# Optimization experiments

Measured on AMD Instinct MI355X. Metric: run time of the kernel, lower is better.

## Reference

```python
import jax, jax.numpy as jnp
import numpy as np

B, S, D_IN, H, G, HD = 1, 2048, 2048, 32, 8, 128
GS = H // G  # group_size = 4
D_OUT = H * HD  # 4096
EPS = 1e-6


def _rmsnorm(x, scale):
    # qwen3-compatible: compute in fp32 over last dim
    xf = x.astype(jnp.float32)
    var = jnp.mean(xf * xf, axis=-1, keepdims=True)
    return (xf * jax.lax.rsqrt(var + EPS) * scale).astype(x.dtype)


def _apply_rope(x, cos, sin):
    # x: [b, h, s, d]; cos/sin: [s, d]
    d2 = x.shape[-1] // 2
    x1, x2 = x[..., :d2], x[..., d2:]
    rotated = jnp.concatenate([-x2, x1], axis=-1)
    return (x * cos[None, None] + rotated * sin[None, None]).astype(x.dtype)


def setup_inputs() -> dict:
    key = jax.random.key(0)
    ks = jax.random.split(key, 8)
    x = jax.random.normal(ks[0], (B, S, D_IN), jnp.float32)
    mask = jnp.triu(jnp.ones((S, S), bool), k=1)  # causal: True = masked
    # RoPE tables [S, HD]
    inv_freq = 1.0 / (10000.0 ** (jnp.arange(0, HD, 2, dtype=jnp.float32) / HD))
    ang = jnp.arange(S, dtype=jnp.float32)[:, None] * inv_freq[None, :]
    ang = jnp.concatenate([ang, ang], axis=-1)
    cos, sin = jnp.cos(ang), jnp.sin(ang)
    std = 0.02
    Wq = jax.random.normal(ks[1], (D_IN, D_OUT), jnp.float32) * std
    Wk = jax.random.normal(ks[2], (D_IN, G * HD), jnp.float32) * std
    Wv = jax.random.normal(ks[3], (D_IN, G * HD), jnp.float32) * std
    Wo = jax.random.normal(ks[4], (D_OUT, D_IN), jnp.float32) * std
    q_scale = jnp.ones((HD,), jnp.float32)
    k_scale = jnp.ones((HD,), jnp.float32)
    return {"x": x, "mask": mask, "cos": cos, "sin": sin,
            "Wq": Wq, "Wk": Wk, "Wv": Wv, "Wo": Wo,
            "q_scale": q_scale, "k_scale": k_scale}


def reference(x, mask, cos, sin, Wq, Wk, Wv, Wo, q_scale, k_scale):
    b, s, _ = x.shape
    q = (x @ Wq).reshape(b, s, H, HD).transpose(0, 2, 1, 3)   # [b,H,s,hd]
    k = (x @ Wk).reshape(b, s, G, HD).transpose(0, 2, 1, 3)   # [b,G,s,hd]
    v = (x @ Wv).reshape(b, s, G, HD).transpose(0, 2, 1, 3)   # [b,G,s,hd]
    q = _rmsnorm(q, q_scale)
    k = _rmsnorm(k, k_scale)
    q = _apply_rope(q, cos[:s], sin[:s])
    k = _apply_rope(k, cos[:s], sin[:s])
    next_k, next_v = k, v  # cache (num_kv_groups heads)
    # GQA via broadcasting instead of repeat_interleave (same math)
    qg = q.reshape(b, G, GS, s, HD)
    scores = jnp.einsum('bgrsd,bgtd->bgrst', qg, k)           # [b,G,gs,s,s]
    scores = jnp.where(mask[None, None, None], -jnp.inf, scores)
    attn = jax.nn.softmax(scores / np.sqrt(HD).astype(np.float32), axis=-1)
    ctx = jnp.einsum('bgrst,bgtd->bgrsd', attn, v)            # [b,G,gs,s,hd]
    ctx = ctx.reshape(b, H, s, HD).transpose(0, 2, 1, 3).reshape(b, s, D_OUT)
    out = ctx @ Wo
    return out, next_k, next_v
```

## Files before the change

kernel.cpp:

```cpp
#include <hip/hip_runtime.h>

typedef unsigned short ushort_t;
typedef short short8 __attribute__((ext_vector_type(8)));
typedef float floatx4 __attribute__((ext_vector_type(4)));

#define S_LEN 2048
#define DIN   2048
#define NH    32
#define NG    8
#define HDIM  128
#define DOUT  4096
#define DKV   1024
#define QLD   6144

__device__ __forceinline__ float b2f(ushort_t u) {
  union { float f; unsigned u; } t; t.u = ((unsigned)u) << 16; return t.f;
}
__device__ __forceinline__ ushort_t f2b(float f) {
  union { float f; unsigned u; } t; t.f = f;
  unsigned v = t.u;
  v += 0x7FFFu + ((v >> 16) & 1u);
  return (ushort_t)(v >> 16);
}

__device__ __forceinline__ void glds16(const ushort_t* g, ushort_t* l) {
  __builtin_amdgcn_global_load_lds((const __attribute__((address_space(1))) void*)g,
                                   (__attribute__((address_space(3))) void*)l, 16, 0, 0);
}

__global__ __launch_bounds__(256) void tcastW(const float* __restrict__ Wq,
                                              const float* __restrict__ Wk,
                                              const float* __restrict__ Wv,
                                              ushort_t* __restrict__ Wt) {
  __shared__ float t[32][33];
  const int x = blockIdx.x;
  const float* W; int N, sx, drow;
  if (x < 128)      { W = Wq; N = DOUT; sx = x * 32;         drow = x * 32; }
  else if (x < 160) { W = Wk; N = DKV;  sx = (x - 128) * 32; drow = 4096 + (x - 128) * 32; }
  else              { W = Wv; N = DKV;  sx = (x - 160) * 32; drow = 5120 + (x - 160) * 32; }
  const int by = blockIdx.y * 32;
  const int tx = threadIdx.x & 31;
  const int ty = threadIdx.x >> 5;
#pragma unroll
  for (int i = 0; i < 32; i += 8)
    t[ty + i][tx] = W[(size_t)(by + ty + i) * N + sx + tx];
  __syncthreads();
#pragma unroll
  for (int i = 0; i < 32; i += 8)
    Wt[(size_t)(drow + ty + i) * DIN + by + tx] = f2b(t[tx][ty + i]);
}

__global__ __launch_bounds__(256) void tcast(const float* __restrict__ W,
                                             ushort_t* __restrict__ Wt,
                                             int N, int ldt) {
  __shared__ float t[32][33];
  const int bx = blockIdx.x * 32;
  const int by = blockIdx.y * 32;
  const int tx = threadIdx.x & 31;
  const int ty = threadIdx.x >> 5;
#pragma unroll
  for (int i = 0; i < 32; i += 8)
    t[ty + i][tx] = W[(size_t)(by + ty + i) * N + bx + tx];
  __syncthreads();
#pragma unroll
  for (int i = 0; i < 32; i += 8)
    Wt[(size_t)(bx + ty + i) * ldt + by + tx] = f2b(t[tx][ty + i]);
}

__global__ __launch_bounds__(256) void castx(const float* __restrict__ x,
                                             ushort_t* __restrict__ xb) {
  const size_t i = ((size_t)blockIdx.x * 256 + threadIdx.x) * 4;
  float4 v = *(const float4*)&x[i];
  union { int2 p; ushort_t s[4]; } w;
  w.s[0] = f2b(v.x); w.s[1] = f2b(v.y); w.s[2] = f2b(v.z); w.s[3] = f2b(v.w);
  *(int2*)&xb[i] = w.p;
}

template <int CF32, int BM>
__global__ __launch_bounds__(256) void gemm_glds(const ushort_t* __restrict__ A, int lda,
                                                 const ushort_t* __restrict__ Bt, int ldb,
                                                 void* __restrict__ Cp, int ldc, int K) {
  constexpr int MI = BM / 32;
  __shared__ __align__(16) ushort_t As[3][BM * 32];
  __shared__ __align__(16) ushort_t Bs[3][4096];
  const int tid  = threadIdx.x;
  const int m0   = blockIdx.y * BM;
  const int n0   = blockIdx.x * 128;
  const int wave = tid >> 6, lane = tid & 63;
  const int lrow = lane & 15, quad = lane >> 4;
  const int wm = (wave >> 1) * (BM / 2), wn = (wave & 1) * 64;

  floatx4 acc[MI][4];
#pragma unroll
  for (int mi = 0; mi < MI; mi++)
#pragma unroll
    for (int ni = 0; ni < 4; ni++)
#pragma unroll
      for (int j = 0; j < 4; j++) acc[mi][ni][j] = 0.0f;

  const int sc = ((tid & 3) ^ ((tid >> 3) & 3)) * 8;
  const ushort_t* ag0 = A + (size_t)(m0 + (tid >> 2)) * lda + sc;
  const ushort_t* ag1 = ag0 + (size_t)64 * lda;
  const ushort_t* bg0 = Bt + (size_t)(n0 + (tid >> 2)) * ldb + sc;
  const ushort_t* bg1 = bg0 + (size_t)64 * ldb;
  const int so = wave * 512;

  auto stage = [&](int k0, ushort_t* aB, ushort_t* bB) {
    glds16(ag0 + k0, aB + so);
    if constexpr (BM == 128) glds16(ag1 + k0, aB + 2048 + so);
    glds16(bg0 + k0, bB + so);
    glds16(bg1 + k0, bB + 2048 + so);
  };

  const int rq = (quad ^ ((lrow >> 1) & 3)) * 8;

  stage(0,  As[0], Bs[0]);
  stage(32, As[1], Bs[1]);
  stage(64, As[2], Bs[2]);

  ushort_t *a_cur = As[0], *a_n1 = As[1], *a_n2 = As[2];
  ushort_t *b_cur = Bs[0], *b_n1 = Bs[1], *b_n2 = Bs[2];

  const int NT = K >> 5;
  for (int t = 0; t < NT; t++) {
    if (t + 2 < NT) {
      if constexpr (BM == 128) asm volatile("s_waitcnt vmcnt(8)" ::: "memory");
      else                     asm volatile("s_waitcnt vmcnt(6)" ::: "memory");
    } else if (t + 1 < NT) {
      if constexpr (BM == 128) asm volatile("s_waitcnt vmcnt(4)" ::: "memory");
      else                     asm volatile("s_waitcnt vmcnt(3)" ::: "memory");
    } else {
      asm volatile("s_waitcnt vmcnt(0)" ::: "memory");
    }
    __builtin_amdgcn_s_barrier();

    short8 af[MI], bfr[4];
#pragma unroll
    for (int mi = 0; mi < MI; mi++)
      af[mi] = *(const short8*)&a_cur[(wm + mi * 16 + lrow) * 32 + rq];
#pragma unroll
    for (int ni = 0; ni < 4; ni++)
      bfr[ni] = *(const short8*)&b_cur[(wn + ni * 16 + lrow) * 32 + rq];
    asm volatile("s_waitcnt lgkmcnt(0)" ::: "memory");
    __builtin_amdgcn_s_barrier();

    if (t + 3 < NT) stage((t + 3) << 5, a_cur, b_cur);

    __builtin_amdgcn_s_setprio(1);
#pragma unroll
    for (int mi = 0; mi < MI; mi++)
#pragma unroll
      for (int ni = 0; ni < 4; ni++)
        acc[mi][ni] = __builtin_amdgcn_mfma_f32_16x16x32_bf16(af[mi], bfr[ni], acc[mi][ni], 0, 0, 0);
    __builtin_amdgcn_s_setprio(0);

    ushort_t* ta = a_cur; a_cur = a_n1; a_n1 = a_n2; a_n2 = ta;
    ushort_t* tb = b_cur; b_cur = b_n1; b_n1 = b_n2; b_n2 = tb;
  }
  asm volatile("s_waitcnt vmcnt(0)" ::: "memory");

#pragma unroll
  for (int mi = 0; mi < MI; mi++)
#pragma unroll
    for (int ni = 0; ni < 4; ni++)
#pragma unroll
      for (int i = 0; i < 4; i++) {
        const int row = m0 + wm + mi * 16 + quad * 4 + i;
        const int col = n0 + wn + ni * 16 + lrow;
        if (CF32) ((float*)Cp)[(size_t)row * ldc + col] = acc[mi][ni][i];
        else      ((ushort_t*)Cp)[(size_t)row * ldc + col] = f2b(acc[mi][ni][i]);
      }
}

__global__ __launch_bounds__(256, 2) void gemm_o(const ushort_t* __restrict__ A, int lda,
                                                 const ushort_t* __restrict__ Bt, int ldb,
                                                 float* __restrict__ C, int ldc, int K) {
  __shared__ __align__(16) ushort_t As[3][64 * 64];
  __shared__ __align__(16) ushort_t Bs[3][128 * 64];
  const int tid  = threadIdx.x;
  const int m0   = blockIdx.y * 64;
  const int n0   = blockIdx.x * 128;
  const int wave = tid >> 6, lane = tid & 63;
  const int lrow = lane & 15, quad = lane >> 4;
  const int wm = (wave >> 1) * 32, wn = (wave & 1) * 64;

  floatx4 acc[2][4];
#pragma unroll
  for (int mi = 0; mi < 2; mi++)
#pragma unroll
    for (int ni = 0; ni < 4; ni++)
#pragma unroll
      for (int j = 0; j < 4; j++) acc[mi][ni][j] = 0.0f;

  const int sc = ((lane & 7) ^ ((lane >> 3) & 7)) * 8;
  const ushort_t* ag = A  + (size_t)(m0 + wave * 8 + (lane >> 3)) * lda + sc;
  const ushort_t* bg = Bt + (size_t)(n0 + wave * 8 + (lane >> 3)) * ldb + sc;

  auto stage = [&](int k0, ushort_t* aB, ushort_t* bB) {
    glds16(ag + k0,                    aB + wave * 512);
    glds16(ag + (size_t)32 * lda + k0, aB + 2048 + wave * 512);
    glds16(bg + k0,                    bB + wave * 512);
    glds16(bg + (size_t)32 * ldb + k0, bB + 2048 + wave * 512);
    glds16(bg + (size_t)64 * ldb + k0, bB + 4096 + wave * 512);
    glds16(bg + (size_t)96 * ldb + k0, bB + 6144 + wave * 512);
  };

  const int rq0 = ((quad)     ^ (lrow & 7)) * 8;
  const int rq1 = ((4 + quad) ^ (lrow & 7)) * 8;

  stage(0,   As[0], Bs[0]);
  stage(64,  As[1], Bs[1]);
  stage(128, As[2], Bs[2]);

  ushort_t *a_cur = As[0], *a_n1 = As[1], *a_n2 = As[2];
  ushort_t *b_cur = Bs[0], *b_n1 = Bs[1], *b_n2 = Bs[2];

  const int NT = K >> 6;
  for (int t = 0; t < NT; t++) {
    if (t + 2 < NT)      asm volatile("s_waitcnt vmcnt(12)" ::: "memory");
    else if (t + 1 < NT) asm volatile("s_waitcnt vmcnt(6)" ::: "memory");
    else                 asm volatile("s_waitcnt vmcnt(0)" ::: "memory");
    __builtin_amdgcn_s_barrier();

    short8 af[2][2], bfr[2][4];
#pragma unroll
    for (int mi = 0; mi < 2; mi++) {
      af[0][mi] = *(const short8*)&a_cur[(wm + mi * 16 + lrow) * 64 + rq0];
      af[1][mi] = *(const short8*)&a_cur[(wm + mi * 16 + lrow) * 64 + rq1];
    }
#pragma unroll
    for (int ni = 0; ni < 4; ni++) {
      bfr[0][ni] = *(const short8*)&b_cur[(wn + ni * 16 + lrow) * 64 + rq0];
      bfr[1][ni] = *(const short8*)&b_cur[(wn + ni * 16 + lrow) * 64 + rq1];
    }
    asm volatile("s_waitcnt lgkmcnt(0)" ::: "memory");
    __builtin_amdgcn_s_barrier();

    if (t + 3 < NT) stage((t + 3) << 6, a_cur, b_cur);

    __builtin_amdgcn_s_setprio(1);
#pragma unroll
    for (int kd = 0; kd < 2; kd++)
#pragma unroll
      for (int mi = 0; mi < 2; mi++)
#pragma unroll
        for (int ni = 0; ni < 4; ni++)
          acc[mi][ni] = __builtin_amdgcn_mfma_f32_16x16x32_bf16(af[kd][mi], bfr[kd][ni], acc[mi][ni], 0, 0, 0);
    __builtin_amdgcn_s_setprio(0);

    ushort_t* ta = a_cur; a_cur = a_n1; a_n1 = a_n2; a_n2 = ta;
    ushort_t* tb = b_cur; b_cur = b_n1; b_n1 = b_n2; b_n2 = tb;
  }
  asm volatile("s_waitcnt vmcnt(0)" ::: "memory");

#pragma unroll
  for (int mi = 0; mi < 2; mi++)
#pragma unroll
    for (int ni = 0; ni < 4; ni++)
#pragma unroll
      for (int i = 0; i < 4; i++) {
        const int row = m0 + wm + mi * 16 + quad * 4 + i;
        const int col = n0 + wn + ni * 16 + lrow;
        C[(size_t)row * ldc + col] = acc[mi][ni][i];
      }
}

__global__ __launch_bounds__(256) void norm_qk(ushort_t* __restrict__ qkv,
                                               const float* __restrict__ cosb,
                                               const float* __restrict__ sinb,
                                               const float* __restrict__ qs,
                                               const float* __restrict__ ks,
                                               ushort_t* __restrict__ kb) {
  const int idx  = blockIdx.x * 4 + (threadIdx.x >> 6);
  const int lane = threadIdx.x & 63;
  const int SH = S_LEN * NH;
  const float QSC = 0.08838834764831845f * 1.4426950408889634f;

  if (idx < SH) {
    const int s = idx >> 5, h = idx & 31;
    ushort_t* row = qkv + (size_t)s * QLD + h * HDIM;
    float x1 = b2f(row[lane]), x2 = b2f(row[lane + 64]);
    float ss = x1 * x1 + x2 * x2;
#pragma unroll
    for (int off = 1; off < 64; off <<= 1) ss += __shfl_xor(ss, off);
    const float inv = rsqrtf(ss * (1.0f / 128.0f) + 1e-6f);
    const float y1 = x1 * inv * qs[lane] * QSC;
    const float y2 = x2 * inv * qs[lane + 64] * QSC;
    const float c1 = cosb[s * HDIM + lane],      s1 = sinb[s * HDIM + lane];
    const float c2 = cosb[s * HDIM + lane + 64], s2 = sinb[s * HDIM + lane + 64];
    row[lane]      = f2b(y1 * c1 - y2 * s1);
    row[lane + 64] = f2b(y2 * c2 + y1 * s2);
  } else {
    const int j = idx - SH;
    const int s = j >> 3, g = j & 7;
    const ushort_t* row = qkv + (size_t)s * QLD + DOUT + g * HDIM;
    float x1 = b2f(row[lane]), x2 = b2f(row[lane + 64]);
    float ss = x1 * x1 + x2 * x2;
#pragma unroll
    for (int off = 1; off < 64; off <<= 1) ss += __shfl_xor(ss, off);
    const float inv = rsqrtf(ss * (1.0f / 128.0f) + 1e-6f);
    const float y1 = x1 * inv * ks[lane];
    const float y2 = x2 * inv * ks[lane + 64];
    const float c1 = cosb[s * HDIM + lane],      s1 = sinb[s * HDIM + lane];
    const float c2 = cosb[s * HDIM + lane + 64], s2 = sinb[s * HDIM + lane + 64];
    ushort_t* o = kb + ((size_t)g * S_LEN + s) * HDIM;
    o[lane]      = f2b(y1 * c1 - y2 * s1);
    o[lane + 64] = f2b(y2 * c2 + y1 * s2);
  }
}

__global__ __launch_bounds__(256) void vtrans(const ushort_t* __restrict__ qkv,
                                              ushort_t* __restrict__ vt) {
  __shared__ ushort_t t[64][65];
  const int g = blockIdx.x;
  const int s0 = blockIdx.y * 64, d0 = blockIdx.z * 64;
  const int tx = threadIdx.x & 63, ty = threadIdx.x >> 6;
#pragma unroll
  for (int i = 0; i < 64; i += 4)
    t[ty + i][tx] = qkv[(size_t)(s0 + ty + i) * QLD + DOUT + DKV + g * HDIM + d0 + tx];
  __syncthreads();
#pragma unroll
  for (int i = 0; i < 64; i += 4)
    vt[((size_t)(g * HDIM + d0 + ty + i)) * S_LEN + s0 + tx] = t[tx][ty + i];
}

__global__ __launch_bounds__(256, 2) void attn(ushort_t* QC,
                                               const ushort_t* __restrict__ Kb,
                                               const ushort_t* __restrict__ Vt) {
  __shared__ __align__(16) ushort_t Ks[2][8192];
  __shared__ __align__(16) ushort_t Vs[2][8192];
  __shared__ __align__(16) ushort_t Ps[64 * 72];
  const int h   = blockIdx.x;
  const int yb  = blockIdx.y;
  const int qtA = 31 - yb;
  const int qtB = yb;
  const int g   = h >> 2;
  const int tid = threadIdx.x;
  const int wave = tid >> 6, lane = tid & 63;
  const int lrow = lane & 15, quad = lane >> 4;
  const ushort_t* Kg = Kb + (size_t)g * S_LEN * HDIM;
  const ushort_t* Vg = Vt + (size_t)g * HDIM * S_LEN;
  const int rA = qtA * 64, rB = qtB * 64;

  short8 qfA[4], qfB[4];
#pragma unroll
  for (int kd = 0; kd < 4; kd++) {
    qfA[kd] = *(const short8*)&QC[(size_t)(rA + wave * 16 + lrow) * QLD + h * HDIM + kd * 32 + quad * 8];
    qfB[kd] = *(const short8*)&QC[(size_t)(rB + wave * 16 + lrow) * QLD + h * HDIM + kd * 32 + quad * 8];
  }

  short8 vones;
#pragma unroll
  for (int j = 0; j < 8; j++) vones[j] = (lrow == 0) ? (short)0x3F80 : (short)0;

  floatx4 ctxA[8], ctxlA, ctxB[8], ctxlB;
#pragma unroll
  for (int nd = 0; nd < 8; nd++)
#pragma unroll
    for (int j = 0; j < 4; j++) { ctxA[nd][j] = 0.0f; ctxB[nd][j] = 0.0f; }
#pragma unroll
  for (int j = 0; j < 4; j++) { ctxlA[j] = 0.0f; ctxlB[j] = 0.0f; }

  const int swz = ((lane & 3) ^ ((lane >> 3) & 3)) * 8;
  const ushort_t* kgl = Kg + (size_t)(wave * 16 + (lane >> 2)) * HDIM + swz;
  const ushort_t* vgl = Vg + (size_t)(wave * 32 + (lane >> 2)) * S_LEN + swz;

  auto stageKV = [&](int t0, int b) {
#pragma unroll
    for (int i = 0; i < 4; i++)
      glds16(kgl + (size_t)t0 * HDIM + i * 32, &Ks[b][i * 2048 + wave * 512]);
#pragma unroll
    for (int i = 0; i < 4; i++)
      glds16(vgl + (size_t)((i >> 1) * 16) * S_LEN + t0 + (i & 1) * 32,
             &Vs[b][(i & 1) * 4096 + (wave * 32 + (i >> 1) * 16) * 32]);
  };

  const int rq = (quad ^ ((lrow >> 1) & 3)) * 8;

  auto qtile = [&](const short8 (&qf)[4], floatx4 (&ctx)[8], floatx4& ctxl,
                   int r0, int t0, const ushort_t* Kc, const ushort_t* Vc) {
    const int qrow0 = r0 + wave * 16;
    floatx4 sacc[4];
#pragma unroll
    for (int ni = 0; ni < 4; ni++)
#pragma unroll
      for (int j = 0; j < 4; j++) sacc[ni][j] = 0.0f;
    __builtin_amdgcn_s_setprio(1);
#pragma unroll
    for (int kd = 0; kd < 4; kd++) {
      short8 kf[4];
#pragma unroll
      for (int ni = 0; ni < 4; ni++)
        kf[ni] = *(const short8*)&Kc[kd * 2048 + (ni * 16 + lrow) * 32 + rq];
#pragma unroll
      for (int ni = 0; ni < 4; ni++)
        sacc[ni] = __builtin_amdgcn_mfma_f32_16x16x32_bf16(qf[kd], kf[ni], sacc[ni], 0, 0, 0);
    }
    __builtin_amdgcn_s_setprio(0);

    const bool diag = (t0 == r0);
#pragma unroll
    for (int ni = 0; ni < 4; ni++)
#pragma unroll
      for (int i = 0; i < 4; i++) {
        float sv = sacc[ni][i];
        if (diag && (t0 + ni * 16 + lrow > qrow0 + quad * 4 + i)) sv = -1e30f;
        sacc[ni][i] = exp2f(sv - 17.0f);
      }

    asm volatile("s_waitcnt lgkmcnt(0)" ::: "memory");
#pragma unroll
    for (int ni = 0; ni < 4; ni++)
#pragma unroll
      for (int i = 0; i < 4; i++)
        Ps[(wave * 16 + quad * 4 + i) * 72 + ni * 16 + lrow] = f2b(sacc[ni][i]);
    asm volatile("s_waitcnt lgkmcnt(0)" ::: "memory");

    __builtin_amdgcn_s_setprio(1);
#pragma unroll
    for (int kt = 0; kt < 2; kt++) {
      const short8 pf = *(const short8*)&Ps[(wave * 16 + lrow) * 72 + kt * 32 + quad * 8];
      ctxl = __builtin_amdgcn_mfma_f32_16x16x32_bf16(pf, vones, ctxl, 0, 0, 0);
#pragma unroll
      for (int nd = 0; nd < 8; nd++) {
        const short8 vf = *(const short8*)&Vc[kt * 4096 + (nd * 16 + lrow) * 32 + rq];
        ctx[nd] = __builtin_amdgcn_mfma_f32_16x16x32_bf16(pf, vf, ctx[nd], 0, 0, 0);
      }
    }
    __builtin_amdgcn_s_setprio(0);
  };

  stageKV(0, 0);
  stageKV(64, 1);

  int buf = 0;
  for (int t = 0; t <= qtA; t++) {
    const int t0 = t * 64;
    if (t < qtA) asm volatile("s_waitcnt vmcnt(8)" ::: "memory");
    else         asm volatile("s_waitcnt vmcnt(0)" ::: "memory");
    __builtin_amdgcn_s_barrier();
    const ushort_t* Kc = Ks[buf];
    const ushort_t* Vc = Vs[buf];

    qtile(qfA, ctxA, ctxlA, rA, t0, Kc, Vc);
    if (t <= qtB) qtile(qfB, ctxB, ctxlB, rB, t0, Kc, Vc);

    asm volatile("s_waitcnt lgkmcnt(0)" ::: "memory");
    __builtin_amdgcn_s_barrier();
    if (t + 2 <= qtA) stageKV((t + 2) * 64, buf);
    buf ^= 1;
  }

  float invlA[4], invlB[4];
#pragma unroll
  for (int i = 0; i < 4; i++) {
    invlA[i] = 1.0f / __shfl(ctxlA[i], lane & 48);
    invlB[i] = 1.0f / __shfl(ctxlB[i], lane & 48);
  }

  asm volatile("s_waitcnt vmcnt(0)" ::: "memory");
  __syncthreads();
  ushort_t* Es = (wave < 2) ? Ks[0] : Vs[0];
  const int eb = (wave & 1) * 16;
  const int erow = lane >> 4;
  const int ecol = (lane & 15) * 8;

#pragma unroll
  for (int i = 0; i < 4; i++)
#pragma unroll
    for (int nd = 0; nd < 8; nd++)
      Es[(eb + quad * 4 + i) * 136 + nd * 16 + lrow] = f2b(ctxA[nd][i] * invlA[i]);
  asm volatile("s_waitcnt lgkmcnt(0)" ::: "memory");
#pragma unroll
  for (int rr = 0; rr < 4; rr++) {
    int4 v = *(const int4*)&Es[(eb + rr * 4 + erow) * 136 + ecol];
    *(int4*)&QC[(size_t)(rA + wave * 16 + rr * 4 + erow) * QLD + h * HDIM + ecol] = v;
  }

  asm volatile("s_waitcnt lgkmcnt(0)" ::: "memory");
#pragma unroll
  for (int i = 0; i < 4; i++)
#pragma unroll
    for (int nd = 0; nd < 8; nd++)
      Es[(eb + quad * 4 + i) * 136 + nd * 16 + lrow] = f2b(ctxB[nd][i] * invlB[i]);
  asm volatile("s_waitcnt lgkmcnt(0)" ::: "memory");
#pragma unroll
  for (int rr = 0; rr < 4; rr++) {
    int4 v = *(const int4*)&Es[(eb + rr * 4 + erow) * 136 + ecol];
    *(int4*)&QC[(size_t)(rB + wave * 16 + rr * 4 + erow) * QLD + h * HDIM + ecol] = v;
  }
}

__global__ __launch_bounds__(256) void fin(const ushort_t* __restrict__ kb,
                                           const ushort_t* __restrict__ qkv,
                                           float* __restrict__ nk,
                                           float* __restrict__ nv) {
  const int bx = blockIdx.x;
  if (bx < 1024) {
    const size_t e = ((size_t)bx * 256 + threadIdx.x) * 8;
    union { int4 v; ushort_t s[8]; } u;
    u.v = *(const int4*)&kb[e];
#pragma unroll
    for (int j = 0; j < 8; j++) nk[e + j] = b2f(u.s[j]);
  } else {
    const int s = bx - 1024;
    const int g = threadIdx.x >> 5, d4 = (threadIdx.x & 31) * 4;
    union { short4 v; ushort_t s[4]; } u;
    u.v = *(const short4*)&qkv[(size_t)s * QLD + DOUT + DKV + g * HDIM + d4];
    float4 o;
    o.x = b2f(u.s[0]); o.y = b2f(u.s[1]); o.z = b2f(u.s[2]); o.w = b2f(u.s[3]);
    *(float4*)&nv[((size_t)g * S_LEN + s) * HDIM + d4] = o;
  }
}

extern "C" void kernel_launch(void* const* d_in, const int* in_sizes, int n_in,
                              void* d_out, int out_size, void* d_ws, size_t ws_size,
                              hipStream_t stream) {
  const float* x    = (const float*)d_in[0];
  const float* cosb = (const float*)d_in[2];
  const float* sinb = (const float*)d_in[3];
  const float* Wq   = (const float*)d_in[4];
  const float* Wk   = (const float*)d_in[5];
  const float* Wv   = (const float*)d_in[6];
  const float* Wo   = (const float*)d_in[7];
  const float* qs   = (const float*)d_in[8];
  const float* ks   = (const float*)d_in[9];

  float* outf = (float*)d_out;
  float* nkf  = outf + (size_t)S_LEN * DIN;
  float* nvf  = nkf + (size_t)NG * S_LEN * HDIM;

  const size_t MiB = 1024 * 1024;
  ushort_t* WallT = (ushort_t*)d_out;
  ushort_t* xb    = (ushort_t*)((char*)d_out + 24 * MiB);
  ushort_t* WoT   = (ushort_t*)((char*)d_out + 16 * MiB);
  ushort_t* vt    = (ushort_t*)d_out;
  ushort_t* qkv   = (ushort_t*)d_ws;
  ushort_t* kb    = (ushort_t*)((char*)d_ws + 24 * MiB);

  tcastW<<<dim3(192, 64), 256, 0, stream>>>(Wq, Wk, Wv, WallT);
  castx<<<4096, 256, 0, stream>>>(x, xb);

  gemm_glds<0, 128><<<dim3(48, 16), 256, 0, stream>>>(xb, DIN, WallT, DIN, qkv, QLD, DIN);

  tcast<<<dim3(64, 128), 256, 0, stream>>>(Wo, WoT, DIN, DOUT);

  norm_qk<<<(S_LEN * NH + S_LEN * NG) / 4, 256, 0, stream>>>(qkv, cosb, sinb, qs, ks, kb);

  vtrans<<<dim3(NG, S_LEN / 64, HDIM / 64), 256, 0, stream>>>(qkv, vt);

  attn<<<dim3(NH, 16), 256, 0, stream>>>(qkv, kb, vt);

  gemm_o<<<dim3(16, 32), 256, 0, stream>>>(qkv, QLD, WoT, DOUT, outf, DIN, DOUT);

  fin<<<3072, 256, 0, stream>>>(kb, qkv, nkf, nvf);
}
```

Before: 361.5 us.

## Merge prep and mid kernels, share K fragments across attention query tiles

The weight-transpose and x-cast kernels are merged into one launch. The Wo transpose, the QK norm/RoPE and the V transpose are merged into a second launch, with each branch chosen by block index. The attention loop now computes the QK^T scores for both query tiles from the same K fragment loads before doing softmax and PV for each, which cuts LDS reads and gives the MFMAs more independent work. The probabilities are packed with v_cvt_pk_bf16_f32, and the fixed -17 exponent offset is dropped, which relies on the normalized scores staying in range.

```diff
diff --git a/kernel.cpp b/kernel.cpp
--- a/kernel.cpp
+++ b/kernel.cpp
@@ -28,52 +28,37 @@
                                    (__attribute__((address_space(3))) void*)l, 16, 0, 0);
 }
 
-__global__ __launch_bounds__(256) void tcastW(const float* __restrict__ Wq,
-                                              const float* __restrict__ Wk,
-                                              const float* __restrict__ Wv,
-                                              ushort_t* __restrict__ Wt) {
+__global__ __launch_bounds__(256) void prep(const float* __restrict__ Wq,
+                                            const float* __restrict__ Wk,
+                                            const float* __restrict__ Wv,
+                                            ushort_t* __restrict__ Wt,
+                                            const float* __restrict__ x,
+                                            ushort_t* __restrict__ xb) {
   __shared__ float t[32][33];
-  const int x = blockIdx.x;
-  const float* W; int N, sx, drow;
-  if (x < 128)      { W = Wq; N = DOUT; sx = x * 32;         drow = x * 32; }
-  else if (x < 160) { W = Wk; N = DKV;  sx = (x - 128) * 32; drow = 4096 + (x - 128) * 32; }
-  else              { W = Wv; N = DKV;  sx = (x - 160) * 32; drow = 5120 + (x - 160) * 32; }
-  const int by = blockIdx.y * 32;
-  const int tx = threadIdx.x & 31;
-  const int ty = threadIdx.x >> 5;
-#pragma unroll
-  for (int i = 0; i < 32; i += 8)
-    t[ty + i][tx] = W[(size_t)(by + ty + i) * N + sx + tx];
-  __syncthreads();
-#pragma unroll
-  for (int i = 0; i < 32; i += 8)
-    Wt[(size_t)(drow + ty + i) * DIN + by + tx] = f2b(t[tx][ty + i]);
-}
-
-__global__ __launch_bounds__(256) void tcast(const float* __restrict__ W,
-                                             ushort_t* __restrict__ Wt,
-                                             int N, int ldt) {
-  __shared__ float t[32][33];
-  const int bx = blockIdx.x * 32;
-  const int by = blockIdx.y * 32;
-  const int tx = threadIdx.x & 31;
-  const int ty = threadIdx.x >> 5;
-#pragma unroll
-  for (int i = 0; i < 32; i += 8)
-    t[ty + i][tx] = W[(size_t)(by + ty + i) * N + bx + tx];
-  __syncthreads();
-#pragma unroll
-  for (int i = 0; i < 32; i += 8)
-    Wt[(size_t)(bx + ty + i) * ldt + by + tx] = f2b(t[tx][ty + i]);
-}
-
-__global__ __launch_bounds__(256) void castx(const float* __restrict__ x,
-                                             ushort_t* __restrict__ xb) {
-  const size_t i = ((size_t)blockIdx.x * 256 + threadIdx.x) * 4;
-  float4 v = *(const float4*)&x[i];
-  union { int2 p; ushort_t s[4]; } w;
-  w.s[0] = f2b(v.x); w.s[1] = f2b(v.y); w.s[2] = f2b(v.z); w.s[3] = f2b(v.w);
-  *(int2*)&xb[i] = w.p;
+  const int bx = blockIdx.x;
+  if (bx < 12288) {
+    const int xi = bx % 192;
+    const int by = (bx / 192) * 32;
+    const float* W; int N, sx, drow;
+    if (xi < 128)      { W = Wq; N = DOUT; sx = xi * 32;         drow = xi * 32; }
+    else if (xi < 160) { W = Wk; N = DKV;  sx = (xi - 128) * 32; drow = 4096 + (xi - 128) * 32; }
+    else               { W = Wv; N = DKV;  sx = (xi - 160) * 32; drow = 5120 + (xi - 160) * 32; }
+    const int tx = threadIdx.x & 31;
+    const int ty = threadIdx.x >> 5;
+#pragma unroll
+    for (int i = 0; i < 32; i += 8)
+      t[ty + i][tx] = W[(size_t)(by + ty + i) * N + sx + tx];
+    __syncthreads();
+#pragma unroll
+    for (int i = 0; i < 32; i += 8)
+      Wt[(size_t)(drow + ty + i) * DIN + by + tx] = f2b(t[tx][ty + i]);
+  } else {
+    const size_t i = ((size_t)(bx - 12288) * 256 + threadIdx.x) * 4;
+    float4 v = *(const float4*)&x[i];
+    union { int2 p; ushort_t s[4]; } w;
+    w.s[0] = f2b(v.x); w.s[1] = f2b(v.y); w.s[2] = f2b(v.z); w.s[3] = f2b(v.w);
+    *(int2*)&xb[i] = w.p;
+  }
 }
 
 template <int CF32, int BM>
@@ -265,63 +250,79 @@
       }
 }
 
-__global__ __launch_bounds__(256) void norm_qk(ushort_t* __restrict__ qkv,
-                                               const float* __restrict__ cosb,
-                                               const float* __restrict__ sinb,
-                                               const float* __restrict__ qs,
-                                               const float* __restrict__ ks,
-                                               ushort_t* __restrict__ kb) {
-  const int idx  = blockIdx.x * 4 + (threadIdx.x >> 6);
-  const int lane = threadIdx.x & 63;
-  const int SH = S_LEN * NH;
-  const float QSC = 0.08838834764831845f * 1.4426950408889634f;
-
-  if (idx < SH) {
-    const int s = idx >> 5, h = idx & 31;
-    ushort_t* row = qkv + (size_t)s * QLD + h * HDIM;
-    float x1 = b2f(row[lane]), x2 = b2f(row[lane + 64]);
-    float ss = x1 * x1 + x2 * x2;
-#pragma unroll
-    for (int off = 1; off < 64; off <<= 1) ss += __shfl_xor(ss, off);
-    const float inv = rsqrtf(ss * (1.0f / 128.0f) + 1e-6f);
-    const float y1 = x1 * inv * qs[lane] * QSC;
-    const float y2 = x2 * inv * qs[lane + 64] * QSC;
-    const float c1 = cosb[s * HDIM + lane],      s1 = sinb[s * HDIM + lane];
-    const float c2 = cosb[s * HDIM + lane + 64], s2 = sinb[s * HDIM + lane + 64];
-    row[lane]      = f2b(y1 * c1 - y2 * s1);
-    row[lane + 64] = f2b(y2 * c2 + y1 * s2);
+__global__ __launch_bounds__(256) void mid(const float* __restrict__ Wo,
+                                           ushort_t* __restrict__ WoT,
+                                           ushort_t* __restrict__ qkv,
+                                           const float* __restrict__ cosb,
+                                           const float* __restrict__ sinb,
+                                           const float* __restrict__ qs,
+                                           const float* __restrict__ ks,
+                                           ushort_t* __restrict__ kb,
+                                           ushort_t* __restrict__ vt) {
+  __shared__ float tf[32][33];
+  __shared__ ushort_t tu[64][65];
+  const int bx = blockIdx.x;
+  if (bx < 8192) {
+    const int bxo = (bx & 63) * 32;
+    const int byo = (bx >> 6) * 32;
+    const int tx = threadIdx.x & 31;
+    const int ty = threadIdx.x >> 5;
+#pragma unroll
+    for (int i = 0; i < 32; i += 8)
+      tf[ty + i][tx] = Wo[(size_t)(byo + ty + i) * DIN + bxo + tx];
+    __syncthreads();
+#pragma unroll
+    for (int i = 0; i < 32; i += 8)
+      WoT[(size_t)(bxo + ty + i) * DOUT + byo + tx] = f2b(tf[tx][ty + i]);
+  } else if (bx < 28672) {
+    const int idx  = (bx - 8192) * 4 + (threadIdx.x >> 6);
+    const int lane = threadIdx.x & 63;
+    const int SH = S_LEN * NH;
+    const float QSC = 0.08838834764831845f * 1.4426950408889634f;
+    if (idx < SH) {
+      const int s = idx >> 5, h = idx & 31;
+      ushort_t* row = qkv + (size_t)s * QLD + h * HDIM;
+      float x1 = b2f(row[lane]), x2 = b2f(row[lane + 64]);
+      float ss = x1 * x1 + x2 * x2;
+#pragma unroll
+      for (int off = 1; off < 64; off <<= 1) ss += __shfl_xor(ss, off);
+      const float inv = rsqrtf(ss * (1.0f / 128.0f) + 1e-6f);
+      const float y1 = x1 * inv * qs[lane] * QSC;
+      const float y2 = x2 * inv * qs[lane + 64] * QSC;
+      const float c1 = cosb[s * HDIM + lane],      s1 = sinb[s * HDIM + lane];
+      const float c2 = cosb[s * HDIM + lane + 64], s2 = sinb[s * HDIM + lane + 64];
+      row[lane]      = f2b(y1 * c1 - y2 * s1);
+      row[lane + 64] = f2b(y2 * c2 + y1 * s2);
+    } else {
+      const int j = idx - SH;
+      const int s = j >> 3, g = j & 7;
+      const ushort_t* row = qkv + (size_t)s * QLD + DOUT + g * HDIM;
+      float x1 = b2f(row[lane]), x2 = b2f(row[lane + 64]);
+      float ss = x1 * x1 + x2 * x2;
+#pragma unroll
+      for (int off = 1; off < 64; off <<= 1) ss += __shfl_xor(ss, off);
+      const float inv = rsqrtf(ss * (1.0f / 128.0f) + 1e-6f);
+      const float y1 = x1 * inv * ks[lane];
+      const float y2 = x2 * inv * ks[lane + 64];
+      const float c1 = cosb[s * HDIM + lane],      s1 = sinb[s * HDIM + lane];
+      const float c2 = cosb[s * HDIM + lane + 64], s2 = sinb[s * HDIM + lane + 64];
+      ushort_t* o = kb + ((size_t)g * S_LEN + s) * HDIM;
+      o[lane]      = f2b(y1 * c1 - y2 * s1);
+      o[lane + 64] = f2b(y2 * c2 + y1 * s2);
+    }
   } else {
-    const int j = idx - SH;
-    const int s = j >> 3, g = j & 7;
-    const ushort_t* row = qkv + (size_t)s * QLD + DOUT + g * HDIM;
-    float x1 = b2f(row[lane]), x2 = b2f(row[lane + 64]);
-    float ss = x1 * x1 + x2 * x2;
-#pragma unroll
-    for (int off = 1; off < 64; off <<= 1) ss += __shfl_xor(ss, off);
-    const float inv = rsqrtf(ss * (1.0f / 128.0f) + 1e-6f);
-    const float y1 = x1 * inv * ks[lane];
-    const float y2 = x2 * inv * ks[lane + 64];
-    const float c1 = cosb[s * HDIM + lane],      s1 = sinb[s * HDIM + lane];
-    const float c2 = cosb[s * HDIM + lane + 64], s2 = sinb[s * HDIM + lane + 64];
-    ushort_t* o = kb + ((size_t)g * S_LEN + s) * HDIM;
-    o[lane]      = f2b(y1 * c1 - y2 * s1);
-    o[lane + 64] = f2b(y2 * c2 + y1 * s2);
-  }
-}
-
-__global__ __launch_bounds__(256) void vtrans(const ushort_t* __restrict__ qkv,
-                                              ushort_t* __restrict__ vt) {
-  __shared__ ushort_t t[64][65];
-  const int g = blockIdx.x;
-  const int s0 = blockIdx.y * 64, d0 = blockIdx.z * 64;
-  const int tx = threadIdx.x & 63, ty = threadIdx.x >> 6;
-#pragma unroll
-  for (int i = 0; i < 64; i += 4)
-    t[ty + i][tx] = qkv[(size_t)(s0 + ty + i) * QLD + DOUT + DKV + g * HDIM + d0 + tx];
-  __syncthreads();
-#pragma unroll
-  for (int i = 0; i < 64; i += 4)
-    vt[((size_t)(g * HDIM + d0 + ty + i)) * S_LEN + s0 + tx] = t[tx][ty + i];
+    const int r = bx - 28672;
+    const int g = r & 7;
+    const int s0 = ((r >> 3) & 31) * 64, d0 = (r >> 8) * 64;
+    const int tx = threadIdx.x & 63, ty = threadIdx.x >> 6;
+#pragma unroll
+    for (int i = 0; i < 64; i += 4)
+      tu[ty + i][tx] = qkv[(size_t)(s0 + ty + i) * QLD + DOUT + DKV + g * HDIM + d0 + tx];
+    __syncthreads();
+#pragma unroll
+    for (int i = 0; i < 64; i += 4)
+      vt[((size_t)(g * HDIM + d0 + ty + i)) * S_LEN + s0 + tx] = tu[tx][ty + i];
+  }
 }
 
 __global__ __launch_bounds__(256, 2) void attn(ushort_t* QC,
@@ -377,45 +378,33 @@
 
   const int rq = (quad ^ ((lrow >> 1) & 3)) * 8;
 
-  auto qtile = [&](const short8 (&qf)[4], floatx4 (&ctx)[8], floatx4& ctxl,
-                   int r0, int t0, const ushort_t* Kc, const ushort_t* Vc) {
+  auto smpack = [&](floatx4 (&s)[4], int r0, int t0) {
     const int qrow0 = r0 + wave * 16;
-    floatx4 sacc[4];
-#pragma unroll
-    for (int ni = 0; ni < 4; ni++)
-#pragma unroll
-      for (int j = 0; j < 4; j++) sacc[ni][j] = 0.0f;
-    __builtin_amdgcn_s_setprio(1);
-#pragma unroll
-    for (int kd = 0; kd < 4; kd++) {
-      short8 kf[4];
-#pragma unroll
-      for (int ni = 0; ni < 4; ni++)
-        kf[ni] = *(const short8*)&Kc[kd * 2048 + (ni * 16 + lrow) * 32 + rq];
-#pragma unroll
-      for (int ni = 0; ni < 4; ni++)
-        sacc[ni] = __builtin_amdgcn_mfma_f32_16x16x32_bf16(qf[kd], kf[ni], sacc[ni], 0, 0, 0);
-    }
-    __builtin_amdgcn_s_setprio(0);
-
     const bool diag = (t0 == r0);
 #pragma unroll
     for (int ni = 0; ni < 4; ni++)
 #pragma unroll
       for (int i = 0; i < 4; i++) {
-        float sv = sacc[ni][i];
+        float sv = s[ni][i];
         if (diag && (t0 + ni * 16 + lrow > qrow0 + quad * 4 + i)) sv = -1e30f;
-        sacc[ni][i] = exp2f(sv - 17.0f);
+        s[ni][i] = exp2f(sv);
       }
-
     asm volatile("s_waitcnt lgkmcnt(0)" ::: "memory");
 #pragma unroll
-    for (int ni = 0; ni < 4; ni++)
-#pragma unroll
-      for (int i = 0; i < 4; i++)
-        Ps[(wave * 16 + quad * 4 + i) * 72 + ni * 16 + lrow] = f2b(sacc[ni][i]);
+    for (int ni = 0; ni < 4; ni++) {
+      unsigned p01, p23;
+      asm volatile("v_cvt_pk_bf16_f32 %0, %1, %2" : "=v"(p01) : "v"(s[ni][0]), "v"(s[ni][1]));
+      asm volatile("v_cvt_pk_bf16_f32 %0, %1, %2" : "=v"(p23) : "v"(s[ni][2]), "v"(s[ni][3]));
+      const int base = (wave * 16 + quad * 4) * 72 + ni * 16 + lrow;
+      Ps[base]       = (ushort_t)(p01 & 0xFFFFu);
+      Ps[base + 72]  = (ushort_t)(p01 >> 16);
+      Ps[base + 144] = (ushort_t)(p23 & 0xFFFFu);
+      Ps[base + 216] = (ushort_t)(p23 >> 16);
+    }
     asm volatile("s_waitcnt lgkmcnt(0)" ::: "memory");
-
+  };
+
+  auto pv = [&](floatx4 (&ctx)[8], floatx4& ctxl, const ushort_t* Vc) {
     __builtin_amdgcn_s_setprio(1);
 #pragma unroll
     for (int kt = 0; kt < 2; kt++) {
@@ -441,9 +430,48 @@
     __builtin_amdgcn_s_barrier();
     const ushort_t* Kc = Ks[buf];
     const ushort_t* Vc = Vs[buf];
-
-    qtile(qfA, ctxA, ctxlA, rA, t0, Kc, Vc);
-    if (t <= qtB) qtile(qfB, ctxB, ctxlB, rB, t0, Kc, Vc);
+    const bool doB = (t <= qtB);
+
+    floatx4 sA[4], sB[4];
+#pragma unroll
+    for (int ni = 0; ni < 4; ni++)
+#pragma unroll
+      for (int j = 0; j < 4; j++) { sA[ni][j] = 0.0f; sB[ni][j] = 0.0f; }
+    __builtin_amdgcn_s_setprio(1);
+    if (doB) {
+#pragma unroll
+      for (int kd = 0; kd < 4; kd++) {
+        short8 kf[4];
+#pragma unroll
+        for (int ni = 0; ni < 4; ni++)
+          kf[ni] = *(const short8*)&Kc[kd * 2048 + (ni * 16 + lrow) * 32 + rq];
+#pragma unroll
+        for (int ni = 0; ni < 4; ni++)
+          sA[ni] = __builtin_amdgcn_mfma_f32_16x16x32_bf16(qfA[kd], kf[ni], sA[ni], 0, 0, 0);
+#pragma unroll
+        for (int ni = 0; ni < 4; ni++)
+          sB[ni] = __builtin_amdgcn_mfma_f32_16x16x32_bf16(qfB[kd], kf[ni], sB[ni], 0, 0, 0);
+      }
+    } else {
+#pragma unroll
+      for (int kd = 0; kd < 4; kd++) {
+        short8 kf[4];
+#pragma unroll
+        for (int ni = 0; ni < 4; ni++)
+          kf[ni] = *(const short8*)&Kc[kd * 2048 + (ni * 16 + lrow) * 32 + rq];
+#pragma unroll
+        for (int ni = 0; ni < 4; ni++)
+          sA[ni] = __builtin_amdgcn_mfma_f32_16x16x32_bf16(qfA[kd], kf[ni], sA[ni], 0, 0, 0);
+      }
+    }
+    __builtin_amdgcn_s_setprio(0);
+
+    smpack(sA, rA, t0);
+    pv(ctxA, ctxlA, Vc);
+    if (doB) {
+      smpack(sB, rB, t0);
+      pv(ctxB, ctxlB, Vc);
+    }
 
     asm volatile("s_waitcnt lgkmcnt(0)" ::: "memory");
     __builtin_amdgcn_s_barrier();
@@ -538,16 +566,11 @@
   ushort_t* qkv   = (ushort_t*)d_ws;
   ushort_t* kb    = (ushort_t*)((char*)d_ws + 24 * MiB);
 
-  tcastW<<<dim3(192, 64), 256, 0, stream>>>(Wq, Wk, Wv, WallT);
-  castx<<<4096, 256, 0, stream>>>(x, xb);
+  prep<<<16384, 256, 0, stream>>>(Wq, Wk, Wv, WallT, x, xb);
 
   gemm_glds<0, 128><<<dim3(48, 16), 256, 0, stream>>>(xb, DIN, WallT, DIN, qkv, QLD, DIN);
 
-  tcast<<<dim3(64, 128), 256, 0, stream>>>(Wo, WoT, DIN, DOUT);
-
-  norm_qk<<<(S_LEN * NH + S_LEN * NG) / 4, 256, 0, stream>>>(qkv, cosb, sinb, qs, ks, kb);
-
-  vtrans<<<dim3(NG, S_LEN / 64, HDIM / 64), 256, 0, stream>>>(qkv, vt);
+  mid<<<29184, 256, 0, stream>>>(Wo, WoT, qkv, cosb, sinb, qs, ks, kb, vt);
 
   attn<<<dim3(NH, 16), 256, 0, stream>>>(qkv, kb, vt);
 
```

After: 344.1 us. -4.8%, faster.
